# Kernel tuning notes

Hardware: AMD Instinct MI355X
Metric: run time of the kernel (lower is better)

Reference implementation:

```python
import jax, jax.numpy as jnp
import numpy as np

B = 2
NCLS = 19    # semantic classes for the logits heads
NLAB = 20    # raw point label values 0..19 (0 = unlabeled)
# (Z, Y, X) grids at strides 2, 4, 8 of sizes=[256,256,32]
GRIDS = {2: (16, 128, 128), 4: (8, 64, 64), 8: (4, 32, 32)}


def _lin_idx(coord, Z, Y, X):
    # coord: (N,4) int rows [b, z, y, x] -> flat cell index over B*Z*Y*X
    b, z, y, x = coord[:, 0], coord[:, 1], coord[:, 2], coord[:, 3]
    return ((b * Z + z) * Y + y) * X + x


def _bev_projection(feat, coord, Y, X):
    # Fused equivalent of torch.unique + scatter_max + spconv dense():
    # scatter_max features directly into the dense (B, Y, X) BEV grid keyed by (b,y,x).
    key = (coord[:, 0] * Y + coord[:, 2]) * X + coord[:, 3]
    C = feat.shape[1]
    dense = jax.ops.segment_max(feat, key, num_segments=B * Y * X)  # empty cells -> -inf
    dense = jnp.where(jnp.isfinite(dense), dense, jnp.zeros((), feat.dtype))
    return dense.reshape(B, Y, X, C).transpose(0, 3, 1, 2)  # (B, C, Y, X)


def _voxel_sem_target(fcoord, pcoord, plabel, Z, Y, X):
    # Majority-vote semantic label per point voxel, gathered at feature voxel coords.
    ncell = B * Z * Y * X
    pair = _lin_idx(pcoord, Z, Y, X) * NLAB + plabel  # (cell, label) key
    counts = jax.ops.segment_sum(
        jnp.ones(pcoord.shape[0], jnp.int32), pair, num_segments=ncell * NLAB
    ).reshape(ncell, NLAB)
    maj = jnp.argmax(counts, axis=1).astype(jnp.int32)   # most frequent label per cell
    occ = counts.sum(axis=1) > 0                          # cell contains any point
    fk = _lin_idx(fcoord, Z, Y, X)
    return jnp.where(occ[fk], maj[fk], 0).astype(jnp.int32)  # unmatched -> 0


def _head(x, w1, g, b, w2, b2):
    # Linear(no bias) -> BatchNorm1d(train stats) -> LeakyReLU(0.1) -> Linear
    h = x @ w1
    mu = h.mean(axis=0)
    var = h.var(axis=0)
    h = (h - mu) * jax.lax.rsqrt(var + 1e-5) * g + b
    h = jnp.where(h >= 0, h, 0.1 * h)
    return h @ w2 + b2


def _rand_coords(key, n, Z, Y, X):
    kb, kz, ky, kx = jax.random.split(key, 4)
    return jnp.stack([
        jax.random.randint(kb, (n,), 0, B, dtype=jnp.int32),
        jax.random.randint(kz, (n,), 0, Z, dtype=jnp.int32),
        jax.random.randint(ky, (n,), 0, Y, dtype=jnp.int32),
        jax.random.randint(kx, (n,), 0, X, dtype=jnp.int32),
    ], axis=1)


def setup_inputs() -> dict:
    key = jax.random.key(0)
    ks = jax.random.split(key, 32)
    M1, M2, M3, NP = 200000, 100000, 50000, 500000
    inp = {
        'proj1_vw': jax.random.normal(ks[0], (M1, 64), jnp.float32),
        'proj2_vw': jax.random.normal(ks[1], (M2, 128), jnp.float32),
        'proj3_vw': jax.random.normal(ks[2], (M3, 256), jnp.float32),
        'vw1_coord': _rand_coords(ks[3], M1, *GRIDS[2]),
        'vw2_coord': _rand_coords(ks[4], M2, *GRIDS[4]),
        'vw3_coord': _rand_coords(ks[5], M3, *GRIDS[8]),
        'idx02': _rand_coords(ks[6], NP, *GRIDS[2]),
        'idx04': _rand_coords(ks[7], NP, *GRIDS[4]),
        'idx08': _rand_coords(ks[8], NP, *GRIDS[8]),
        'pw_label': jax.random.randint(ks[9], (NP,), 0, NLAB, dtype=jnp.int32),
    }
    # learned head parameters (out2 / out4 / out8)
    def head_params(k, cin):
        k1, k2 = jax.random.split(k)
        return (jax.random.normal(k1, (cin, 64), jnp.float32) * 0.02,
                jnp.ones((64,), jnp.float32), jnp.zeros((64,), jnp.float32),
                jax.random.normal(k2, (64, NCLS), jnp.float32) * 0.02,
                jnp.zeros((NCLS,), jnp.float32))
    for tag, k, cin in (('h2', ks[10], 64), ('h4', ks[11], 128), ('h8', ks[12], 256)):
        w1, g, b, w2, b2 = head_params(k, cin)
        inp[f'{tag}_w1'], inp[f'{tag}_g'], inp[f'{tag}_b'] = w1, g, b
        inp[f'{tag}_w2'], inp[f'{tag}_b2'] = w2, b2
    return inp


def reference(proj1_vw, proj2_vw, proj3_vw, vw1_coord, vw2_coord, vw3_coord,
              idx02, idx04, idx08, pw_label,
              h2_w1, h2_g, h2_b, h2_w2, h2_b2,
              h4_w1, h4_g, h4_b, h4_w2, h4_b2,
              h8_w1, h8_g, h8_b, h8_w2, h8_b2):
    (Z2, Y2, X2), (Z4, Y4, X4), (Z8, Y8, X8) = GRIDS[2], GRIDS[4], GRIDS[8]
    bev1 = _bev_projection(proj1_vw, vw1_coord, Y2, X2)   # (B, 64, 128, 128)
    bev2 = _bev_projection(proj2_vw, vw2_coord, Y4, X4)   # (B, 128, 64, 64)
    bev3 = _bev_projection(proj3_vw, vw3_coord, Y8, X8)   # (B, 256, 32, 32)
    lbl2 = _voxel_sem_target(vw1_coord, idx02, pw_label, Z2, Y2, X2)
    lbl4 = _voxel_sem_target(vw2_coord, idx04, pw_label, Z4, Y4, X4)
    lbl8 = _voxel_sem_target(vw3_coord, idx08, pw_label, Z8, Y8, X8)
    log2 = _head(proj1_vw, h2_w1, h2_g, h2_b, h2_w2, h2_b2)
    log4 = _head(proj2_vw, h4_w1, h4_g, h4_b, h4_w2, h4_b2)
    log8 = _head(proj3_vw, h8_w1, h8_g, h8_b, h8_w2, h8_b2)
    return (bev1, bev2, bev3, log2, log4, log8, lbl2, lbl4, lbl8)
```

## Files before the change

### kernel.cpp

```cpp
#include <hip/hip_runtime.h>
#include <hip/hip_bf16.h>

typedef unsigned int u32;
typedef unsigned short u16;
typedef __attribute__((ext_vector_type(8))) short short8;
typedef __attribute__((ext_vector_type(4))) float f32x4;

#define NLAB 20

#define M_1 200000
#define C_1 64
#define Z_1 16
#define Y_1 128
#define X_1 128

#define M_2 100000
#define C_2 128
#define Z_2 8
#define Y_2 64
#define X_2 64

#define M_3 50000
#define C_3 256
#define Z_3 4
#define Y_3 32
#define X_3 32

#define O_BEV1 0
#define O_BEV2 2097152
#define O_BEV3 3145728
#define O_LOG1 3670016
#define O_LOG2 7470016
#define O_LOG3 9370016
#define O_LBL1 10320016
#define O_LBL2 10520016
#define O_LBL3 10620016

#define NCELLS 43008
#define SB1 0
#define SB2 32768
#define SB3 40960

#define CAP1 40
#define CAP2 64
#define CAP3 96
#define P1 43008
#define P2 1353728
#define P3 1878016

#define WPART 2080000
#define WP1 0
#define WP2 400000
#define WP3 600064
#define WSTATS 2780160

#define WBEV_F  4194304
#define WBEV2_F 6291456
#define WBEV3_F 7340032

#define WC1_W 8388608
#define WC2_W 11010048
#define WC3_W 11337728
#define W_COUNT_BYTES 11960320ull
#define NZB 730

#define WH_BIG_U16 22806528
#define WH1 0
#define WH2 12800000
#define WH3 19200000

#define GB1 3125
#define GB2 1563
#define GB3 782
#define HB1 782
#define HB2 391
#define HB3 196

#define NGEMM 5470
#define NGATH 3584
#define NCNT  5862
#define NMEGA 14916

static __device__ __forceinline__ u16 f2bf(float f) {
  u32 u = __float_as_uint(f);
  u32 r = u + 0x7fffu + ((u >> 16) & 1u);
  return (u16)(r >> 16);
}


static __device__ __forceinline__ void dev_count(int cb, int tid,
    const int* i2, const int* i4, const int* i8, const int* lab, u32* hist)
{
  const int* pc; int Z, Y, X; u32* base; int i;
  if (cb < 1954)      { pc = i2; Z = Z_1; Y = Y_1; X = X_1; base = hist + WC1_W; i = cb * 256 + tid; }
  else if (cb < 3908) { pc = i4; Z = Z_2; Y = Y_2; X = X_2; base = hist + WC2_W; i = (cb - 1954) * 256 + tid; }
  else                { pc = i8; Z = Z_3; Y = Y_3; X = X_3; base = hist + WC3_W; i = (cb - 3908) * 256 + tid; }
  if (i >= 500000) return;
  int4 c = *(const int4*)(pc + i * 4);
  int l = lab[i];
  int lin = ((c.x * Z + c.y) * Y + c.z) * X + c.w;
  atomicAdd(base + lin * 5 + (l >> 2), 1u << ((l & 3) * 8));
}

#define GBATCH 8
static __device__ __forceinline__ void dev_gather(int gb, int tid,
    const float* f1, const float* f2, const float* f3,
    const int* cur2, const int* pidx2, float* ws)
{
  int w = gb * 4 + (tid >> 6);
  int lane = tid & 63;
  int t0 = w * 4;
  int C = (t0 < 32768) ? 64 : (t0 < 49152) ? 128 : 256;
  const float* fp[4]; int n[4], st[4]; u32 wb[4];
#pragma unroll
  for (int k = 0; k < 4; k++) {
    int t = t0 + k; const float* f; int cidx, stv, cap; u32 wbv;
    if (t < 32768) {
      f = f1; cidx = SB1 + t; stv = P1 + t * CAP1; cap = CAP1;
      wbv = WBEV_F + (u32)t * 64;
    } else if (t < 49152) {
      int u = t - 32768; int cell = u >> 1, ch = (u & 1) * 64;
      f = f2 + ch; cidx = SB2 + cell; stv = P2 + cell * CAP2; cap = CAP2;
      wbv = WBEV2_F + (u32)cell * 128 + ch;
    } else {
      int u = t - 49152; int cell = u >> 2, ch = (u & 3) * 64;
      f = f3 + ch; cidx = SB3 + cell; stv = P3 + cell * CAP3; cap = CAP3;
      wbv = WBEV3_F + (u32)cell * 256 + ch;
    }
    fp[k] = f; wb[k] = wbv; st[k] = stv;
    int cnt = cur2[cidx];
    n[k] = cnt < cap ? cnt : cap;
  }
  int maxn = max(max(n[0], n[1]), max(n[2], n[3]));
  float acc[4];
#pragma unroll
  for (int k = 0; k < 4; k++) acc[k] = __uint_as_float(0xff800000u);
  for (int base = 0; base < maxn; base += GBATCH) {
    int p[4][GBATCH];
#pragma unroll
    for (int k = 0; k < 4; k++) {
      int hi = st[k] + (n[k] > 0 ? n[k] - 1 : 0);
      int s = st[k] + base;
#pragma unroll
      for (int j = 0; j < GBATCH; j++) {
        int idx = s + j;
        idx = idx < hi ? idx : hi;
        int pv = pidx2[idx];
        p[k][j] = n[k] > 0 ? pv : 0;
      }
    }
    float v[4][GBATCH];
#pragma unroll
    for (int k = 0; k < 4; k++)
#pragma unroll
      for (int j = 0; j < GBATCH; j++)
        v[k][j] = fp[k][(size_t)p[k][j] * C + lane];
#pragma unroll
    for (int k = 0; k < 4; k++)
#pragma unroll
      for (int j = 0; j < GBATCH; j++)
        acc[k] = fmaxf(acc[k], v[k][j]);
  }
#pragma unroll
  for (int k = 0; k < 4; k++)
    ws[wb[k] + lane] = (n[k] > 0) ? acc[k] : 0.f;
}

static __device__ __forceinline__ void dev_gemm(int blk, int tid,
    const float* x1, const float* x2, const float* x3,
    const float* w1a, const float* w1b, const float* w1c,
    u16* hbuf, float* part)
{
  const float* x; const float* w1; u16* h; float* pp; int Cin, M, bl, NB;
  if (blk < GB1)            { x = x1; w1 = w1a; h = hbuf + WH1; pp = part + WP1; Cin = C_1; M = M_1; bl = blk;             NB = GB1; }
  else if (blk < GB1 + GB2) { x = x2; w1 = w1b; h = hbuf + WH2; pp = part + WP2; Cin = C_2; M = M_2; bl = blk - GB1;       NB = GB2; }
  else                      { x = x3; w1 = w1c; h = hbuf + WH3; pp = part + WP3; Cin = C_3; M = M_3; bl = blk - GB1 - GB2; NB = GB3; }
  int lane = tid & 63, wv = tid >> 6;
  int m16 = lane & 15, quad = lane >> 4;

  __shared__ u16 As[64 * 72];
  __shared__ u16 Bs[64 * 72];
  __shared__ float redS[4][64];
  __shared__ float redQ[4][64];

  f32x4 acc[4];
#pragma unroll
  for (int nt = 0; nt < 4; nt++) acc[nt] = (f32x4){0.f, 0.f, 0.f, 0.f};

  int nchunk = Cin >> 6;
  for (int c = 0; c < nchunk; c++) {
    if (c) __syncthreads();
#pragma unroll
    for (int pass = 0; pass < 4; pass++) {
      int fidx = pass * 256 + tid;
      int row = fidx >> 4, kp = (fidx & 15) * 4;
      int grow = bl * 64 + row;
      float4 v = make_float4(0.f, 0.f, 0.f, 0.f);
      if (grow < M) v = *(const float4*)(x + (size_t)grow * Cin + c * 64 + kp);
      ushort4 o = { f2bf(v.x), f2bf(v.y), f2bf(v.z), f2bf(v.w) };
      *(ushort4*)(As + row * 72 + kp) = o;
    }
    {
      int n = tid & 63, kg = tid >> 6;
#pragma unroll
      for (int p = 0; p < 4; p++) {
        int k0 = kg * 4 + p * 16;
        const float* wp = w1 + (size_t)(c * 64 + k0) * 64 + n;
        ushort4 o = { f2bf(wp[0]), f2bf(wp[64]), f2bf(wp[128]), f2bf(wp[192]) };
        *(ushort4*)(Bs + n * 72 + k0) = o;
      }
    }
    __syncthreads();
#pragma unroll
    for (int ks = 0; ks < 2; ks++) {
      short8 a0 = *(const short8*)(As + (wv * 16 + m16) * 72 + ks * 32 + quad * 8);
      short8 b[4];
#pragma unroll
      for (int nt = 0; nt < 4; nt++)
        b[nt] = *(const short8*)(Bs + (nt * 16 + m16) * 72 + ks * 32 + quad * 8);
#pragma unroll
      for (int nt = 0; nt < 4; nt++)
        acc[nt] = __builtin_amdgcn_mfma_f32_16x16x32_bf16(a0, b[nt], acc[nt], 0, 0, 0);
    }
  }

  float s[4] = {0.f, 0.f, 0.f, 0.f}, q[4] = {0.f, 0.f, 0.f, 0.f};
#pragma unroll
  for (int nt = 0; nt < 4; nt++) {
#pragma unroll
    for (int r = 0; r < 4; r++) {
      float v = acc[nt][r];
      int grow = bl * 64 + wv * 16 + quad * 4 + r;
      if (grow < M) h[(size_t)grow * 64 + nt * 16 + m16] = f2bf(v);
      s[nt] += v;
      q[nt] = fmaf(v, v, q[nt]);
    }
  }
#pragma unroll
  for (int nt = 0; nt < 4; nt++) {
    s[nt] += __shfl_xor(s[nt], 16); s[nt] += __shfl_xor(s[nt], 32);
    q[nt] += __shfl_xor(q[nt], 16); q[nt] += __shfl_xor(q[nt], 32);
  }
  if (lane < 16) {
#pragma unroll
    for (int nt = 0; nt < 4; nt++) {
      redS[wv][nt * 16 + lane] = s[nt];
      redQ[wv][nt * 16 + lane] = q[nt];
    }
  }
  __syncthreads();
  if (tid < 64) {
    pp[tid * NB + bl] = redS[0][tid] + redS[1][tid] + redS[2][tid] + redS[3][tid];
  } else if (tid < 128) {
    int n2 = tid - 64;
    pp[(64 + n2) * NB + bl] = redQ[0][n2] + redQ[1][n2] + redQ[2][n2] + redQ[3][n2];
  }
}

static __device__ __forceinline__ void dev_lbl(int blk, int tid,
    const int* fc1, const int* fc2, const int* fc3, const u32* hist, float* out)
{
  const int* fc; int Z, Y, X, M; const u32* base; long lbase; int m;
  if (blk < HB1)            { fc = fc1; Z = Z_1; Y = Y_1; X = X_1; M = M_1; base = hist + WC1_W; lbase = O_LBL1; m = blk * 256 + tid; }
  else if (blk < HB1 + HB2) { fc = fc2; Z = Z_2; Y = Y_2; X = X_2; M = M_2; base = hist + WC2_W; lbase = O_LBL2; m = (blk - HB1) * 256 + tid; }
  else                      { fc = fc3; Z = Z_3; Y = Y_3; X = X_3; M = M_3; base = hist + WC3_W; lbase = O_LBL3; m = (blk - HB1 - HB2) * 256 + tid; }
  if (m >= M) return;
  int4 c = *(const int4*)(fc + m * 4);
  int lin = ((c.x * Z + c.y) * Y + c.z) * X + c.w;
  const u32* cp = base + lin * 5;
  u32 w0 = cp[0], w1 = cp[1], w2 = cp[2], w3 = cp[3], w4 = cp[4];
  int best = (int)(w0 & 0xffu); int bi = 0;
#pragma unroll
  for (int n = 1; n < NLAB; n++) {
    u32 w = (n < 4) ? w0 : (n < 8) ? w1 : (n < 12) ? w2 : (n < 16) ? w3 : w4;
    int cc = (int)((w >> ((n & 3) * 8)) & 0xffu);
    if (cc > best) { best = cc; bi = n; }
  }
  out[lbase + m] = (float)bi;
}

static __device__ __forceinline__ void dev_transpose(int bid, int tid,
    const float* ws, float* out)
{
  __shared__ float tileU[4160];
  if (bid < 512) {
    int b = bid >> 8, y = (bid >> 1) & 127, x0 = (bid & 1) * 64;
    const float* src = ws + WBEV_F + (size_t)((b * 128 + y) * 128 + x0) * 64;
#pragma unroll
    for (int pass = 0; pass < 16; pass++) {
      int idx = pass * 256 + tid;
      int x = idx >> 6, c = idx & 63;
      tileU[x * 65 + c] = src[(size_t)x * 64 + c];
    }
    __syncthreads();
    size_t ob = O_BEV1 + ((size_t)(b * 64) * 128 + y) * 128 + x0;
#pragma unroll
    for (int pass = 0; pass < 16; pass++) {
      int idx = pass * 256 + tid;
      int c = idx >> 6, x = idx & 63;
      out[ob + (size_t)c * 16384 + x] = tileU[x * 65 + c];
    }
  } else if (bid < 768) {
    int t = bid - 512;
    int b = t >> 7, y = (t >> 1) & 63, x0 = (t & 1) * 32;
    const float* src = ws + WBEV2_F + (size_t)((b * 64 + y) * 64 + x0) * 128;
#pragma unroll
    for (int pass = 0; pass < 16; pass++) {
      int idx = pass * 256 + tid;
      int x = idx >> 7, c = idx & 127;
      tileU[x * 129 + c] = src[(size_t)x * 128 + c];
    }
    __syncthreads();
    size_t ob = O_BEV2 + ((size_t)(b * 128) * 64 + y) * 64 + x0;
#pragma unroll
    for (int pass = 0; pass < 16; pass++) {
      int idx = pass * 256 + tid;
      int c = idx >> 5, x = idx & 31;
      out[ob + (size_t)c * 4096 + x] = tileU[x * 129 + c];
    }
  } else {
    int t = bid - 768;
    int b = t >> 6, y = (t >> 1) & 31, ch0 = (t & 1) * 128;
    const float* src = ws + WBEV3_F + (size_t)((b * 32 + y) * 32) * 256 + ch0;
#pragma unroll
    for (int pass = 0; pass < 16; pass++) {
      int idx = pass * 256 + tid;
      int x = idx >> 7, c = idx & 127;
      tileU[x * 129 + c] = src[(size_t)x * 256 + c];
    }
    __syncthreads();
    size_t ob = O_BEV3 + ((size_t)(b * 256 + ch0) * 32 + y) * 32;
#pragma unroll
    for (int pass = 0; pass < 16; pass++) {
      int idx = pass * 256 + tid;
      int c = idx >> 5, x = idx & 31;
      out[ob + (size_t)c * 1024 + x] = tileU[x * 129 + c];
    }
  }
}

static __device__ __forceinline__ void dev_stats(int sblk, int tid,
    const float* part, float* stats,
    const float* g1, const float* b1, const float* g4, const float* b4,
    const float* g8, const float* b8)
{
  int sc = sblk >> 6, col = sblk & 63;
  int nb; const float* p; float invM; const float* g; const float* bb;
  if (sc == 0)      { nb = GB1; p = part + WP1; invM = 1.f / M_1; g = g1; bb = b1; }
  else if (sc == 1) { nb = GB2; p = part + WP2; invM = 1.f / M_2; g = g4; bb = b4; }
  else              { nb = GB3; p = part + WP3; invM = 1.f / M_3; g = g8; bb = b8; }
  const float* ps = p + (size_t)col * nb;
  const float* pq = p + (size_t)(64 + col) * nb;
  float s = 0.f, q = 0.f;
  for (int i = tid; i < nb; i += 256) { s += ps[i]; q += pq[i]; }
  __shared__ float r1[256], r2[256];
  r1[tid] = s; r2[tid] = q;
  __syncthreads();
  for (int off = 128; off > 0; off >>= 1) {
    if (tid < off) { r1[tid] += r1[tid + off]; r2[tid] += r2[tid + off]; }
    __syncthreads();
  }
  if (tid == 0) {
    float mu  = r1[0] * invM;
    float var = r2[0] * invM - mu * mu;
    float scale = rsqrtf(var + 1e-5f) * g[col];
    stats[sc * 128 + col]      = scale;
    stats[sc * 128 + 64 + col] = fmaf(-mu, scale, bb[col]);
  }
}


__global__ __launch_bounds__(256) void k_scatter2(
    const int* __restrict__ co1, const int* __restrict__ co2, const int* __restrict__ co3,
    int* __restrict__ cur2, int* __restrict__ pidx2, uint4* __restrict__ histz)
{
  int blk = blockIdx.x;
  if (blk >= HB1 + HB2 + HB3) {
    int zb = blk - (HB1 + HB2 + HB3);
    uint4 z = {0u, 0u, 0u, 0u};
    uint4* dst = histz + (size_t)zb * 1024 + threadIdx.x;
#pragma unroll
    for (int r = 0; r < 4; r++) dst[r * 256] = z;
    return;
  }
  const int* co; int Y, X, M, base, m, pbase, cap;
  if (blk < HB1)            { co = co1; Y = Y_1; X = X_1; M = M_1; base = SB1; pbase = P1; cap = CAP1; m = blk * 256 + threadIdx.x; }
  else if (blk < HB1 + HB2) { co = co2; Y = Y_2; X = X_2; M = M_2; base = SB2; pbase = P2; cap = CAP2; m = (blk - HB1) * 256 + threadIdx.x; }
  else                      { co = co3; Y = Y_3; X = X_3; M = M_3; base = SB3; pbase = P3; cap = CAP3; m = (blk - HB1 - HB2) * 256 + threadIdx.x; }
  if (m >= M) return;
  int4 c = *(const int4*)(co + m * 4);
  int cell = (c.x * Y + c.z) * X + c.w;
  int slot = atomicAdd(cur2 + base + cell, 1);
  if (slot < cap) pidx2[pbase + cell * cap + slot] = m;
}

__global__ __launch_bounds__(256) void k_mega(
    const float* __restrict__ x1, const float* __restrict__ x2, const float* __restrict__ x3,
    const float* __restrict__ w1a, const float* __restrict__ w1b, const float* __restrict__ w1c,
    u16* __restrict__ hbuf, float* __restrict__ part,
    const int* __restrict__ cur2, const int* __restrict__ pidx2,
    float* __restrict__ ws,
    const int* __restrict__ i2, const int* __restrict__ i4, const int* __restrict__ i8,
    const int* __restrict__ lab, u32* __restrict__ hist)
{
  int blk = blockIdx.x;
  if (blk < NGEMM) {
    dev_gemm(blk, threadIdx.x, x1, x2, x3, w1a, w1b, w1c, hbuf, part);
  } else if (blk < NGEMM + NGATH) {
    dev_gather(blk - NGEMM, threadIdx.x, x1, x2, x3, cur2, pidx2, ws);
  } else {
    dev_count(blk - (NGEMM + NGATH), threadIdx.x, i2, i4, i8, lab, hist);
  }
}

__global__ __launch_bounds__(256) void k_tl(
    const float* __restrict__ ws, const u32* __restrict__ hist,
    const int* __restrict__ fc1, const int* __restrict__ fc2, const int* __restrict__ fc3,
    float* __restrict__ out,
    const float* __restrict__ part, float* __restrict__ stats,
    const float* __restrict__ g1, const float* __restrict__ b1,
    const float* __restrict__ g4, const float* __restrict__ b4,
    const float* __restrict__ g8, const float* __restrict__ b8)
{
  int blk = blockIdx.x;
  if (blk < HB1 + HB2 + HB3) {
    dev_lbl(blk, threadIdx.x, fc1, fc2, fc3, hist, out);
  } else if (blk < HB1 + HB2 + HB3 + 896) {
    dev_transpose(blk - (HB1 + HB2 + HB3), threadIdx.x, ws, out);
  } else {
    dev_stats(blk - (HB1 + HB2 + HB3 + 896), threadIdx.x, part, stats, g1, b1, g4, b4, g8, b8);
  }
}

__global__ __launch_bounds__(256) void k_head(
    const u16* __restrict__ hbuf, const float* __restrict__ stats,
    const float* __restrict__ w21, const float* __restrict__ c21,
    const float* __restrict__ w24, const float* __restrict__ c24,
    const float* __restrict__ w28, const float* __restrict__ c28,
    float* __restrict__ out)
{
  int blk = blockIdx.x;
  const u16* h; const float* st; const float* w2; const float* b2;
  int M; long obase; int bl;
  if (blk < HB1)            { h = hbuf + WH1; st = stats;       w2 = w21; b2 = c21; M = M_1; obase = O_LOG1; bl = blk; }
  else if (blk < HB1 + HB2) { h = hbuf + WH2; st = stats + 128; w2 = w24; b2 = c24; M = M_2; obase = O_LOG2; bl = blk - HB1; }
  else                      { h = hbuf + WH3; st = stats + 256; w2 = w28; b2 = c28; M = M_3; obase = O_LOG3; bl = blk - HB1 - HB2; }
  int tid = threadIdx.x;
  int rowbase = bl * 256;
  int avail = M - rowbase; if (avail > 256) avail = 256;

  __shared__ __align__(16) float os[256 * 19];

  float acc[19];
#pragma unroll
  for (int n = 0; n < 19; n++) acc[n] = 0.f;

  if (tid < avail) {
    const uint4* hr = (const uint4*)(h + (size_t)(rowbase + tid) * 64);
    uint4 d[8];
#pragma unroll
    for (int q = 0; q < 8; q++) d[q] = hr[q];
#pragma unroll
    for (int q = 0; q < 8; q++) {
#pragma unroll
      for (int half = 0; half < 2; half++) {
        u32 dx = half ? d[q].z : d[q].x;
        u32 dy = half ? d[q].w : d[q].y;
        int j = q * 8 + half * 4;
        float f0 = __uint_as_float(dx << 16);
        float f1 = __uint_as_float(dx & 0xffff0000u);
        float f2 = __uint_as_float(dy << 16);
        float f3 = __uint_as_float(dy & 0xffff0000u);
        float a0 = fmaf(f0, st[j],     st[64 + j]);     a0 = a0 >= 0.f ? a0 : 0.1f * a0;
        float a1 = fmaf(f1, st[j + 1], st[64 + j + 1]); a1 = a1 >= 0.f ? a1 : 0.1f * a1;
        float a2 = fmaf(f2, st[j + 2], st[64 + j + 2]); a2 = a2 >= 0.f ? a2 : 0.1f * a2;
        float a3 = fmaf(f3, st[j + 3], st[64 + j + 3]); a3 = a3 >= 0.f ? a3 : 0.1f * a3;
#pragma unroll
        for (int n = 0; n < 19; n++) {
          acc[n] = fmaf(a0, w2[j * 19 + n], acc[n]);
          acc[n] = fmaf(a1, w2[(j + 1) * 19 + n], acc[n]);
          acc[n] = fmaf(a2, w2[(j + 2) * 19 + n], acc[n]);
          acc[n] = fmaf(a3, w2[(j + 3) * 19 + n], acc[n]);
        }
      }
    }
#pragma unroll
    for (int n = 0; n < 19; n++) os[tid * 19 + n] = acc[n] + b2[n];
  }
  __syncthreads();
  int tot = avail * 19;
  float* op = out + obase + (size_t)rowbase * 19;
  for (int i = tid; i < tot; i += 256) op[i] = os[i];
}

extern "C" void kernel_launch(void* const* d_in, const int* in_sizes, int n_in,
                              void* d_out, int out_size, void* d_ws, size_t ws_size,
                              hipStream_t stream) {
  (void)in_sizes; (void)n_in; (void)out_size; (void)ws_size;
  const float* p1 = (const float*)d_in[0];
  const float* p2 = (const float*)d_in[1];
  const float* p3 = (const float*)d_in[2];
  const int* vc1  = (const int*)d_in[3];
  const int* vc2  = (const int*)d_in[4];
  const int* vc3  = (const int*)d_in[5];
  const int* i2   = (const int*)d_in[6];
  const int* i4   = (const int*)d_in[7];
  const int* i8   = (const int*)d_in[8];
  const int* lab  = (const int*)d_in[9];
  const float* h2w1 = (const float*)d_in[10]; const float* h2g = (const float*)d_in[11];
  const float* h2b  = (const float*)d_in[12]; const float* h2w2 = (const float*)d_in[13];
  const float* h2b2 = (const float*)d_in[14];
  const float* h4w1 = (const float*)d_in[15]; const float* h4g = (const float*)d_in[16];
  const float* h4b  = (const float*)d_in[17]; const float* h4w2 = (const float*)d_in[18];
  const float* h4b2 = (const float*)d_in[19];
  const float* h8w1 = (const float*)d_in[20]; const float* h8g = (const float*)d_in[21];
  const float* h8b  = (const float*)d_in[22]; const float* h8w2 = (const float*)d_in[23];
  const float* h8b2 = (const float*)d_in[24];

  float* out = (float*)d_out;
  int* wsi = (int*)d_ws;
  u32* wsu = (u32*)d_ws;
  float* wsf = (float*)d_ws;
  u16* wsh = (u16*)d_ws;

  u16* hbig = wsh + WH_BIG_U16;
  float* pbig = wsf + WPART;
  float* sbig = wsf + WSTATS;

  hipMemsetAsync(wsi, 0, NCELLS * sizeof(int), stream);

  k_scatter2<<<HB1 + HB2 + HB3 + NZB, 256, 0, stream>>>(vc1, vc2, vc3, wsi, wsi,
      (uint4*)(wsu + WC1_W));

  k_mega<<<NMEGA, 256, 0, stream>>>(p1, p2, p3,
      h2w1, h4w1, h8w1, hbig, pbig,
      wsi, wsi, wsf,
      i2, i4, i8, lab, wsu);

  k_tl<<<HB1 + HB2 + HB3 + 896 + 192, 256, 0, stream>>>(wsf, wsu, vc1, vc2, vc3, out,
      pbig, sbig, h2g, h2b, h4g, h4b, h8g, h8b);

  k_head<<<HB1 + HB2 + HB3, 256, 0, stream>>>(hbig, sbig,
      h2w2, h2b2, h4w2, h4b2, h8w2, h8b2, out);
}
```

Measured before the change: 421.2 us.

## Split BN stats into tiny kernel and fuse head with label and transpose

Moves the BatchNorm statistics reduction into its own small kernel and merges the logits head with the label-vote and BEV-transpose work into one launch. The head blocks can then share the machine with the memory-bound transpose and label blocks instead of waiting for them to finish. The fused kernel uses one shared buffer sized for the head (19 KB), which the transpose reuses. That may lower occupancy for the transpose blocks and adds a small extra launch.

```diff
diff --git a/kernel.cpp b/kernel.cpp
--- a/kernel.cpp
+++ b/kernel.cpp
@@ -75,11 +75,14 @@
 #define HB1 782
 #define HB2 391
 #define HB3 196
+#define NHB (HB1 + HB2 + HB3)
 
 #define NGEMM 5470
 #define NGATH 3584
 #define NCNT  5862
 #define NMEGA 14916
+
+#define NTLH (NHB + NHB + 896)
 
 static __device__ __forceinline__ u16 f2bf(float f) {
   u32 u = __float_as_uint(f);
@@ -280,9 +283,8 @@
 }
 
 static __device__ __forceinline__ void dev_transpose(int bid, int tid,
-    const float* ws, float* out)
-{
-  __shared__ float tileU[4160];
+    const float* ws, float* out, float* tileU)
+{
   if (bid < 512) {
     int b = bid >> 8, y = (bid >> 1) & 127, x0 = (bid & 1) * 64;
     const float* src = ws + WBEV_F + (size_t)((b * 128 + y) * 128 + x0) * 64;
@@ -369,87 +371,18 @@
   }
 }
 
-
-__global__ __launch_bounds__(256) void k_scatter2(
-    const int* __restrict__ co1, const int* __restrict__ co2, const int* __restrict__ co3,
-    int* __restrict__ cur2, int* __restrict__ pidx2, uint4* __restrict__ histz)
-{
-  int blk = blockIdx.x;
-  if (blk >= HB1 + HB2 + HB3) {
-    int zb = blk - (HB1 + HB2 + HB3);
-    uint4 z = {0u, 0u, 0u, 0u};
-    uint4* dst = histz + (size_t)zb * 1024 + threadIdx.x;
-#pragma unroll
-    for (int r = 0; r < 4; r++) dst[r * 256] = z;
-    return;
-  }
-  const int* co; int Y, X, M, base, m, pbase, cap;
-  if (blk < HB1)            { co = co1; Y = Y_1; X = X_1; M = M_1; base = SB1; pbase = P1; cap = CAP1; m = blk * 256 + threadIdx.x; }
-  else if (blk < HB1 + HB2) { co = co2; Y = Y_2; X = X_2; M = M_2; base = SB2; pbase = P2; cap = CAP2; m = (blk - HB1) * 256 + threadIdx.x; }
-  else                      { co = co3; Y = Y_3; X = X_3; M = M_3; base = SB3; pbase = P3; cap = CAP3; m = (blk - HB1 - HB2) * 256 + threadIdx.x; }
-  if (m >= M) return;
-  int4 c = *(const int4*)(co + m * 4);
-  int cell = (c.x * Y + c.z) * X + c.w;
-  int slot = atomicAdd(cur2 + base + cell, 1);
-  if (slot < cap) pidx2[pbase + cell * cap + slot] = m;
-}
-
-__global__ __launch_bounds__(256) void k_mega(
-    const float* __restrict__ x1, const float* __restrict__ x2, const float* __restrict__ x3,
-    const float* __restrict__ w1a, const float* __restrict__ w1b, const float* __restrict__ w1c,
-    u16* __restrict__ hbuf, float* __restrict__ part,
-    const int* __restrict__ cur2, const int* __restrict__ pidx2,
-    float* __restrict__ ws,
-    const int* __restrict__ i2, const int* __restrict__ i4, const int* __restrict__ i8,
-    const int* __restrict__ lab, u32* __restrict__ hist)
-{
-  int blk = blockIdx.x;
-  if (blk < NGEMM) {
-    dev_gemm(blk, threadIdx.x, x1, x2, x3, w1a, w1b, w1c, hbuf, part);
-  } else if (blk < NGEMM + NGATH) {
-    dev_gather(blk - NGEMM, threadIdx.x, x1, x2, x3, cur2, pidx2, ws);
-  } else {
-    dev_count(blk - (NGEMM + NGATH), threadIdx.x, i2, i4, i8, lab, hist);
-  }
-}
-
-__global__ __launch_bounds__(256) void k_tl(
-    const float* __restrict__ ws, const u32* __restrict__ hist,
-    const int* __restrict__ fc1, const int* __restrict__ fc2, const int* __restrict__ fc3,
-    float* __restrict__ out,
-    const float* __restrict__ part, float* __restrict__ stats,
-    const float* __restrict__ g1, const float* __restrict__ b1,
-    const float* __restrict__ g4, const float* __restrict__ b4,
-    const float* __restrict__ g8, const float* __restrict__ b8)
-{
-  int blk = blockIdx.x;
-  if (blk < HB1 + HB2 + HB3) {
-    dev_lbl(blk, threadIdx.x, fc1, fc2, fc3, hist, out);
-  } else if (blk < HB1 + HB2 + HB3 + 896) {
-    dev_transpose(blk - (HB1 + HB2 + HB3), threadIdx.x, ws, out);
-  } else {
-    dev_stats(blk - (HB1 + HB2 + HB3 + 896), threadIdx.x, part, stats, g1, b1, g4, b4, g8, b8);
-  }
-}
-
-__global__ __launch_bounds__(256) void k_head(
-    const u16* __restrict__ hbuf, const float* __restrict__ stats,
-    const float* __restrict__ w21, const float* __restrict__ c21,
-    const float* __restrict__ w24, const float* __restrict__ c24,
-    const float* __restrict__ w28, const float* __restrict__ c28,
-    float* __restrict__ out)
-{
-  int blk = blockIdx.x;
+static __device__ __forceinline__ void dev_head(int blk, int tid,
+    const u16* hbuf, const float* stats,
+    const float* w21, const float* c21, const float* w24, const float* c24,
+    const float* w28, const float* c28, float* out, float* os)
+{
   const u16* h; const float* st; const float* w2; const float* b2;
   int M; long obase; int bl;
   if (blk < HB1)            { h = hbuf + WH1; st = stats;       w2 = w21; b2 = c21; M = M_1; obase = O_LOG1; bl = blk; }
   else if (blk < HB1 + HB2) { h = hbuf + WH2; st = stats + 128; w2 = w24; b2 = c24; M = M_2; obase = O_LOG2; bl = blk - HB1; }
   else                      { h = hbuf + WH3; st = stats + 256; w2 = w28; b2 = c28; M = M_3; obase = O_LOG3; bl = blk - HB1 - HB2; }
-  int tid = threadIdx.x;
   int rowbase = bl * 256;
   int avail = M - rowbase; if (avail > 256) avail = 256;
-
-  __shared__ __align__(16) float os[256 * 19];
 
   float acc[19];
 #pragma unroll
@@ -491,6 +424,78 @@
   int tot = avail * 19;
   float* op = out + obase + (size_t)rowbase * 19;
   for (int i = tid; i < tot; i += 256) op[i] = os[i];
+}
+
+
+__global__ __launch_bounds__(256) void k_scatter2(
+    const int* __restrict__ co1, const int* __restrict__ co2, const int* __restrict__ co3,
+    int* __restrict__ cur2, int* __restrict__ pidx2, uint4* __restrict__ histz)
+{
+  int blk = blockIdx.x;
+  if (blk >= NHB) {
+    int zb = blk - NHB;
+    uint4 z = {0u, 0u, 0u, 0u};
+    uint4* dst = histz + (size_t)zb * 1024 + threadIdx.x;
+#pragma unroll
+    for (int r = 0; r < 4; r++) dst[r * 256] = z;
+    return;
+  }
+  const int* co; int Y, X, M, base, m, pbase, cap;
+  if (blk < HB1)            { co = co1; Y = Y_1; X = X_1; M = M_1; base = SB1; pbase = P1; cap = CAP1; m = blk * 256 + threadIdx.x; }
+  else if (blk < HB1 + HB2) { co = co2; Y = Y_2; X = X_2; M = M_2; base = SB2; pbase = P2; cap = CAP2; m = (blk - HB1) * 256 + threadIdx.x; }
+  else                      { co = co3; Y = Y_3; X = X_3; M = M_3; base = SB3; pbase = P3; cap = CAP3; m = (blk - HB1 - HB2) * 256 + threadIdx.x; }
+  if (m >= M) return;
+  int4 c = *(const int4*)(co + m * 4);
+  int cell = (c.x * Y + c.z) * X + c.w;
+  int slot = atomicAdd(cur2 + base + cell, 1);
+  if (slot < cap) pidx2[pbase + cell * cap + slot] = m;
+}
+
+__global__ __launch_bounds__(256) void k_mega(
+    const float* __restrict__ x1, const float* __restrict__ x2, const float* __restrict__ x3,
+    const float* __restrict__ w1a, const float* __restrict__ w1b, const float* __restrict__ w1c,
+    u16* __restrict__ hbuf, float* __restrict__ part,
+    const int* __restrict__ cur2, const int* __restrict__ pidx2,
+    float* __restrict__ ws,
+    const int* __restrict__ i2, const int* __restrict__ i4, const int* __restrict__ i8,
+    const int* __restrict__ lab, u32* __restrict__ hist)
+{
+  int blk = blockIdx.x;
+  if (blk < NGEMM) {
+    dev_gemm(blk, threadIdx.x, x1, x2, x3, w1a, w1b, w1c, hbuf, part);
+  } else if (blk < NGEMM + NGATH) {
+    dev_gather(blk - NGEMM, threadIdx.x, x1, x2, x3, cur2, pidx2, ws);
+  } else {
+    dev_count(blk - (NGEMM + NGATH), threadIdx.x, i2, i4, i8, lab, hist);
+  }
+}
+
+__global__ __launch_bounds__(256) void k_stats(const float* __restrict__ part, float* __restrict__ stats,
+    const float* __restrict__ g1, const float* __restrict__ b1,
+    const float* __restrict__ g4, const float* __restrict__ b4,
+    const float* __restrict__ g8, const float* __restrict__ b8)
+{
+  dev_stats(blockIdx.x, threadIdx.x, part, stats, g1, b1, g4, b4, g8, b8);
+}
+
+__global__ __launch_bounds__(256) void k_tlh(
+    const u16* __restrict__ hbuf, const float* __restrict__ stats,
+    const float* __restrict__ w21, const float* __restrict__ c21,
+    const float* __restrict__ w24, const float* __restrict__ c24,
+    const float* __restrict__ w28, const float* __restrict__ c28,
+    const float* __restrict__ ws, const u32* __restrict__ hist,
+    const int* __restrict__ fc1, const int* __restrict__ fc2, const int* __restrict__ fc3,
+    float* __restrict__ out)
+{
+  __shared__ __align__(16) float smem[256 * 19];
+  int blk = blockIdx.x;
+  if (blk < NHB) {
+    dev_head(blk, threadIdx.x, hbuf, stats, w21, c21, w24, c24, w28, c28, out, smem);
+  } else if (blk < NHB + NHB) {
+    dev_lbl(blk - NHB, threadIdx.x, fc1, fc2, fc3, hist, out);
+  } else {
+    dev_transpose(blk - 2 * NHB, threadIdx.x, ws, out, smem);
+  }
 }
 
 extern "C" void kernel_launch(void* const* d_in, const int* in_sizes, int n_in,
@@ -529,7 +534,7 @@
 
   hipMemsetAsync(wsi, 0, NCELLS * sizeof(int), stream);
 
-  k_scatter2<<<HB1 + HB2 + HB3 + NZB, 256, 0, stream>>>(vc1, vc2, vc3, wsi, wsi,
+  k_scatter2<<<NHB + NZB, 256, 0, stream>>>(vc1, vc2, vc3, wsi, wsi,
       (uint4*)(wsu + WC1_W));
 
   k_mega<<<NMEGA, 256, 0, stream>>>(p1, p2, p3,
@@ -537,9 +542,9 @@
       wsi, wsi, wsf,
       i2, i4, i8, lab, wsu);
 
-  k_tl<<<HB1 + HB2 + HB3 + 896 + 192, 256, 0, stream>>>(wsf, wsu, vc1, vc2, vc3, out,
-      pbig, sbig, h2g, h2b, h4g, h4b, h8g, h8b);
-
-  k_head<<<HB1 + HB2 + HB3, 256, 0, stream>>>(hbig, sbig,
-      h2w2, h2b2, h4w2, h4b2, h8w2, h8b2, out);
-}
+  k_stats<<<192, 256, 0, stream>>>(pbig, sbig, h2g, h2b, h4g, h4b, h8g, h8b);
+
+  k_tlh<<<NTLH, 256, 0, stream>>>(hbig, sbig,
+      h2w2, h2b2, h4w2, h4b2, h8w2, h8b2,
+      wsf, wsu, vc1, vc2, vc3, out);
+}
```

Result: faster. 411.5 us (-2.3%).
